# Kernel tuning notes

Hardware: AMD Instinct MI355X
Metric: run time of the kernel (lower is better)

Reference implementation:

```python
import jax, jax.numpy as jnp
import numpy as np
import math

D = 2048
H = 32
HKV = 8
HD = D // H
ROPE_BASE = 10000.0


def _rope_cache(T, hd, base=ROPE_BASE):
    theta = 1.0 / base ** (jnp.arange(0, hd, 2, dtype=jnp.float32) / hd)  # [hd//2]
    t = jnp.arange(T, dtype=jnp.float32)
    freqs = t[:, None] * theta[None, :]  # [T, hd//2]
    return jnp.cos(freqs), jnp.sin(freqs)


def _apply_rope(x, cos, sin):
    # x: [B, H, T, HD]; interleaved-pair rotation
    B, Hh, T, hd = x.shape
    x_ = x.reshape(B, Hh, T, hd // 2, 2)
    x1, x2 = x_[..., 0], x_[..., 1]
    c = cos[None, None, :, :]
    s = sin[None, None, :, :]
    rx1 = x1 * c - x2 * s
    rx2 = x1 * s + x2 * c
    return jnp.stack([rx1, rx2], axis=-1).reshape(B, Hh, T, hd)


def setup_inputs() -> dict:
    key = jax.random.key(0)
    ks = jax.random.split(key, 5)
    B, T = 1, 2048
    sc = 0.02
    return {
        "x": jax.random.normal(ks[0], (B, T, D), dtype=jnp.float32),
        "wq": jax.random.normal(ks[1], (D, D), dtype=jnp.float32) * sc,
        "wk": jax.random.normal(ks[2], (HKV * HD, D), dtype=jnp.float32) * sc,
        "wv": jax.random.normal(ks[3], (HKV * HD, D), dtype=jnp.float32) * sc,
        "wo": jax.random.normal(ks[4], (D, D), dtype=jnp.float32) * sc,
    }


def reference(x, wq, wk, wv, wo):
    B, T, _ = x.shape
    q = (x @ wq.T).reshape(B, T, H, HD).transpose(0, 2, 1, 3)      # [B,H,T,HD]
    k = (x @ wk.T).reshape(B, T, HKV, HD).transpose(0, 2, 1, 3)    # [B,HKV,T,HD]
    v = (x @ wv.T).reshape(B, T, HKV, HD).transpose(0, 2, 1, 3)

    cos, sin = _rope_cache(T, HD)
    q = _apply_rope(q, cos, sin)
    k = _apply_rope(k, cos, sin)

    rep = H // HKV
    k = jnp.repeat(k, rep, axis=1)  # repeat_interleave over head dim
    v = jnp.repeat(v, rep, axis=1)

    scores = jnp.einsum("bhtd,bhsd->bhts", q, k) / math.sqrt(HD)
    mask = jnp.triu(jnp.full((T, T), -jnp.inf, dtype=scores.dtype), k=1)
    scores = scores + mask[None, None, :, :]
    attn = jax.nn.softmax(scores, axis=-1)

    y = jnp.einsum("bhts,bhsd->bhtd", attn, v)
    y = y.transpose(0, 2, 1, 3).reshape(B, T, D)
    return y @ wo.T
```

## Files before the change

kernel.cpp:

```cpp
#include <hip/hip_runtime.h>
#include <hip/hip_bf16.h>
#include <cstdint>
#include <cstddef>

#define TT 2048
#define DDIM 2048
#define NH 32
#define NKV 8
#define HDIM 64

typedef __attribute__((ext_vector_type(8))) short bf16x8;
typedef __attribute__((ext_vector_type(4))) float f32x4;
typedef __attribute__((ext_vector_type(16))) float f32x16;

__device__ __forceinline__ unsigned short f2bf(float f) {
  unsigned u = __float_as_uint(f);
  unsigned r = 0x7FFFu + ((u >> 16) & 1u);
  return (unsigned short)((u + r) >> 16);
}
__device__ __forceinline__ float bf2f(unsigned short u) {
  return __uint_as_float((unsigned)u << 16);
}

__device__ __forceinline__ void gl_lds16(const void* g, void* l) {
  __builtin_amdgcn_global_load_lds(
      (const __attribute__((address_space(1))) void*)g,
      (__attribute__((address_space(3))) void*)l, 16, 0, 0);
}

__device__ __forceinline__ unsigned pkbf(float lo, float hi) {
  unsigned r;
  asm("v_cvt_pk_bf16_f32 %0, %1, %2" : "=v"(r) : "v"(lo), "v"(hi));
  return r;
}
__device__ __forceinline__ void swap32(unsigned& dst, unsigned& src) {
  asm volatile("v_permlane32_swap_b32 %0, %1" : "+v"(dst), "+v"(src));
}
union W4 { unsigned w[4]; bf16x8 v; };

__global__ __launch_bounds__(256)
void cast5_kernel(const float* __restrict__ x, const float* __restrict__ wq,
                  const float* __restrict__ wk, const float* __restrict__ wv,
                  const float* __restrict__ wo,
                  unsigned short* __restrict__ xb, unsigned short* __restrict__ wqb,
                  unsigned short* __restrict__ wkb, unsigned short* __restrict__ wvb,
                  unsigned short* __restrict__ wob) {
  int i = blockIdx.x * 256 + threadIdx.x;
  const float* s; unsigned short* d; int off;
  if (i < 1048576)      { s = x;  d = xb;  off = i; }
  else if (i < 2097152) { s = wq; d = wqb; off = i - 1048576; }
  else if (i < 2359296) { s = wk; d = wkb; off = i - 2097152; }
  else if (i < 2621440) { s = wv; d = wvb; off = i - 2359296; }
  else                  { s = wo; d = wob; off = i - 2621440; }
  float4 f = reinterpret_cast<const float4*>(s)[off];
  ushort4 o;
  o.x = f2bf(f.x); o.y = f2bf(f.y); o.z = f2bf(f.z); o.w = f2bf(f.w);
  reinterpret_cast<ushort4*>(d)[off] = o;
}

__device__ __forceinline__ void gemm64_body(
    const unsigned short* __restrict__ A, const unsigned short* __restrict__ B,
    int K, size_t arow, size_t brow,
    unsigned short (*As)[64 * 64], unsigned short (*Bs)[128 * 64],
    f32x4 (&acc)[2][4]) {
  const int tid = threadIdx.x;
  const int wave = tid >> 6, lane = tid & 63;
  const int wm = wave >> 1, wn = wave & 1;
  const int lr = lane & 15;
  const int gb = lane >> 4;
  const int srow = lane >> 3;
  const int scol = (((lane & 7) ^ srow) << 3);

#define G64_STAGE(buf, k0)                                                       \
  {                                                                              \
    for (int i = 0; i < 2; ++i) {                                                \
      int blk = wave * 2 + i;                                                    \
      int r = blk * 8 + srow;                                                    \
      gl_lds16(A + arow + (size_t)r * K + (k0) + scol, &As[buf][blk * 8 * 64]);  \
    }                                                                            \
    for (int i = 0; i < 4; ++i) {                                                \
      int blk = wave * 4 + i;                                                    \
      int r = blk * 8 + srow;                                                    \
      gl_lds16(B + brow + (size_t)r * K + (k0) + scol, &Bs[buf][blk * 8 * 64]);  \
    }                                                                            \
  }

  const int nt = K >> 6;
  G64_STAGE(0, 0)
  __syncthreads();
  int cur = 0;
  for (int t = 0; t < nt; ++t) {
    if (t + 1 < nt) { G64_STAGE(cur ^ 1, (t + 1) << 6) }

    bf16x8 af[2][2], bfr[2][4];
    for (int mi = 0; mi < 2; ++mi) {
      int row = wm * 32 + mi * 16 + lr, sw = row & 7;
      af[0][mi] = *reinterpret_cast<const bf16x8*>(&As[cur][row * 64 + ((gb ^ sw) << 3)]);
      af[1][mi] = *reinterpret_cast<const bf16x8*>(&As[cur][row * 64 + (((4 + gb) ^ sw) << 3)]);
    }
    for (int ni = 0; ni < 4; ++ni) {
      int row = wn * 64 + ni * 16 + lr, sw = row & 7;
      bfr[0][ni] = *reinterpret_cast<const bf16x8*>(&Bs[cur][row * 64 + ((gb ^ sw) << 3)]);
      bfr[1][ni] = *reinterpret_cast<const bf16x8*>(&Bs[cur][row * 64 + (((4 + gb) ^ sw) << 3)]);
    }
    __builtin_amdgcn_s_setprio(1);
    for (int kk = 0; kk < 2; ++kk)
      for (int mi = 0; mi < 2; ++mi)
        for (int ni = 0; ni < 4; ++ni)
          acc[mi][ni] = __builtin_amdgcn_mfma_f32_16x16x32_bf16(af[kk][mi], bfr[kk][ni], acc[mi][ni], 0, 0, 0);
    __builtin_amdgcn_s_setprio(0);
    __syncthreads();
    cur ^= 1;
  }
#undef G64_STAGE
}

__global__ __launch_bounds__(256, 3)
void qkv_fused_kernel(const unsigned short* __restrict__ xb,
                      const unsigned short* __restrict__ wqb,
                      const unsigned short* __restrict__ wkb,
                      const unsigned short* __restrict__ wvb,
                      unsigned short* __restrict__ qhb,
                      unsigned short* __restrict__ khb,
                      unsigned short* __restrict__ vtb) {
  __shared__ __align__(16) unsigned short As[2][64 * 64];
  __shared__ __align__(16) unsigned short Bs[2][128 * 64];
  const int bn = blockIdx.y;
  const unsigned short* B; int n0, mode;
  if (bn < 16)      { B = wqb; n0 = bn;      mode = 0; }
  else if (bn < 20) { B = wkb; n0 = bn - 16; mode = 1; }
  else              { B = wvb; n0 = bn - 20; mode = 2; }

  f32x4 acc[2][4];
  for (int i = 0; i < 2; ++i)
    for (int j = 0; j < 4; ++j)
      acc[i][j] = (f32x4){0.f, 0.f, 0.f, 0.f};

  gemm64_body(xb, B, 2048, (size_t)(blockIdx.x * 64) * 2048,
              (size_t)(n0 * 128) * 2048, As, Bs, acc);

  const int tid = threadIdx.x;
  const int wave = tid >> 6, lane = tid & 63;
  const int wm = wave >> 1, wn = wave & 1;
  const int lr = lane & 15;

  if (mode == 2) {
#pragma unroll
    for (int mi = 0; mi < 2; ++mi)
#pragma unroll
      for (int ni = 0; ni < 4; ++ni) {
        int n = n0 * 128 + wn * 64 + ni * 16 + lr;
        int tb = blockIdx.x * 64 + wm * 32 + mi * 16 + (lane >> 4) * 4;
        ushort4 u;
        u.x = f2bf(acc[mi][ni][0]); u.y = f2bf(acc[mi][ni][1]);
        u.z = f2bf(acc[mi][ni][2]); u.w = f2bf(acc[mi][ni][3]);
        *reinterpret_cast<ushort4*>(&vtb[(size_t)n * TT + tb]) = u;
      }
  } else {
    unsigned short* dst = (mode == 0) ? qhb : khb;
    const float scale = (mode == 0) ? 0.18033688011112042f : 1.0f;
#pragma unroll
    for (int mi = 0; mi < 2; ++mi)
#pragma unroll
      for (int ni = 0; ni < 4; ++ni) {
        int n = n0 * 128 + wn * 64 + ni * 16 + lr;
        int hh = n >> 6, d = n & 63, ii = d >> 1;
        float theta = exp2f(-(float)(2 * ii) * (13.287712379549449f / 64.0f));
        int tb = blockIdx.x * 64 + wm * 32 + mi * 16 + (lane >> 4) * 4;
#pragma unroll
        for (int r = 0; r < 4; ++r) {
          float self = acc[mi][ni][r];
          float part = __shfl_xor(self, 1);
          float sn, cs;
          __sincosf((float)(tb + r) * theta, &sn, &cs);
          float val = (d & 1) ? (part * sn + self * cs) : (self * cs - part * sn);
          dst[((size_t)hh * TT + tb + r) * HDIM + d] = f2bf(val * scale);
        }
      }
  }
}

__global__ __launch_bounds__(256, 3)
void out_gemm_kernel(const unsigned short* __restrict__ yb,
                     const unsigned short* __restrict__ wob,
                     float* __restrict__ out) {
  __shared__ __align__(16) unsigned short As[2][64 * 64];
  __shared__ __align__(16) unsigned short Bs[2][128 * 64];
  f32x4 acc[2][4];
  for (int i = 0; i < 2; ++i)
    for (int j = 0; j < 4; ++j)
      acc[i][j] = (f32x4){0.f, 0.f, 0.f, 0.f};

  gemm64_body(yb, wob, 2048, (size_t)(blockIdx.x * 64) * 2048,
              (size_t)(blockIdx.y * 128) * 2048, As, Bs, acc);

  const int tid = threadIdx.x;
  const int wave = tid >> 6, lane = tid & 63;
  const int wm = wave >> 1, wn = wave & 1;
  const int lr = lane & 15;
#pragma unroll
  for (int mi = 0; mi < 2; ++mi)
#pragma unroll
    for (int ni = 0; ni < 4; ++ni) {
      int col = blockIdx.y * 128 + wn * 64 + ni * 16 + lr;
      int rbase = blockIdx.x * 64 + wm * 32 + mi * 16 + (lane >> 4) * 4;
#pragma unroll
      for (int r = 0; r < 4; ++r)
        out[(size_t)(rbase + r) * DDIM + col] = acc[mi][ni][r];
    }
}

__global__ __launch_bounds__(256)
void attn_kernel(const unsigned short* __restrict__ qh,
                 const unsigned short* __restrict__ kh,
                 const unsigned short* __restrict__ vt,
                 unsigned short* __restrict__ po,
                 float* __restrict__ pm, float* __restrict__ pl) {
  __shared__ __align__(16) unsigned short Ks[2][64 * 64];
  __shared__ __align__(16) unsigned short Vts[2][64 * 64];
  const int kvg = blockIdx.x;
  const int by = blockIdx.y;
  const int qt = 63 - (by >> 1);
  const int par = by & 1;
  const int tid = threadIdx.x, wave = tid >> 6, lane = tid & 63;
  const int h = kvg * 4 + wave;
  const int qc = lane & 31, hi = lane >> 5;
  const int srow = lane >> 3;
  const int scol = (((lane & 7) ^ srow) << 3);

  bf16x8 qa[4];
  {
    const unsigned short* qrow = qh + ((size_t)h * TT + qt * 32 + qc) * HDIM + hi * 8;
#pragma unroll
    for (int ks = 0; ks < 4; ++ks)
      qa[ks] = *reinterpret_cast<const bf16x8*>(qrow + ks * 16);
  }

  f32x16 oA, oB;
#pragma unroll
  for (int r = 0; r < 16; ++r) { oA[r] = 0.f; oB[r] = 0.f; }
  float m_r = -1e30f, l_r = 0.f;

  const int njb = (qt >> 1) + 1;
  const int cnt = (njb - par + 1) >> 1;

#define A_STAGE(buf, jbx) do {                                                        \
    for (int i = 0; i < 2; ++i) {                                                     \
      int rblk = wave * 2 + i;                                                        \
      int rr = rblk * 8 + srow;                                                       \
      gl_lds16(kh + ((size_t)kvg * TT + (size_t)(jbx) * 64 + rr) * HDIM + scol,       \
               &Ks[buf][rblk * 8 * 64]);                                              \
      gl_lds16(vt + ((size_t)(kvg * HDIM + rr)) * TT + (size_t)(jbx) * 64 + scol,     \
               &Vts[buf][rblk * 8 * 64]);                                             \
    } } while (0)

  if (cnt > 0) {
    A_STAGE(0, par);
    __syncthreads();
    int cur = 0;

    for (int it = 0; it < cnt; ++it) {
      const int jb = par + 2 * it;
      if (it + 1 < cnt) A_STAGE(cur ^ 1, jb + 2);
      const bool diag = (jb == njb - 1);
      const bool hasB = (!diag) || (qt & 1);

      f32x16 stA, stB;
#pragma unroll
      for (int r = 0; r < 16; ++r) { stA[r] = 0.f; stB[r] = 0.f; }
      __builtin_amdgcn_s_setprio(1);
#pragma unroll
      for (int ks = 0; ks < 4; ++ks) {
        int row = qc, g = 2 * ks + hi;
        bf16x8 kf = *reinterpret_cast<const bf16x8*>(&Ks[cur][row * 64 + ((g ^ (row & 7)) << 3)]);
        stA = __builtin_amdgcn_mfma_f32_32x32x16_bf16(kf, qa[ks], stA, 0, 0, 0);
      }
      if (hasB) {
#pragma unroll
        for (int ks = 0; ks < 4; ++ks) {
          int row = 32 + qc, g = 2 * ks + hi;
          bf16x8 kf = *reinterpret_cast<const bf16x8*>(&Ks[cur][row * 64 + ((g ^ (row & 7)) << 3)]);
          stB = __builtin_amdgcn_mfma_f32_32x32x16_bf16(kf, qa[ks], stB, 0, 0, 0);
        }
      }
      __builtin_amdgcn_s_setprio(0);

      if (diag) {
        if (qt & 1) {
#pragma unroll
          for (int r = 0; r < 16; ++r) {
            int jloc = (r & 3) + 8 * (r >> 2) + 4 * hi;
            stB[r] = (jloc > qc) ? -1e30f : stB[r];
          }
        } else {
#pragma unroll
          for (int r = 0; r < 16; ++r) {
            int jloc = (r & 3) + 8 * (r >> 2) + 4 * hi;
            stA[r] = (jloc > qc) ? -1e30f : stA[r];
          }
        }
      }

      float pmx = stA[0];
#pragma unroll
      for (int r = 1; r < 16; ++r) pmx = fmaxf(pmx, stA[r]);
      if (hasB) {
#pragma unroll
        for (int r = 0; r < 16; ++r) pmx = fmaxf(pmx, stB[r]);
      }
      pmx = fmaxf(pmx, __shfl_xor(pmx, 32));
      if (!__all(pmx <= m_r + 12.f)) {
        float mn = fmaxf(m_r, pmx);
        float al = exp2f(m_r - mn);
        m_r = mn; l_r *= al;
#pragma unroll
        for (int r = 0; r < 16; ++r) {
          int qrow = (r & 3) + 8 * (r >> 2) + 4 * hi;
          float alr = __shfl(al, qrow);
          oA[r] *= alr; oB[r] *= alr;
        }
      }
      float sum = 0.f;
#pragma unroll
      for (int r = 0; r < 16; ++r) { stA[r] = exp2f(stA[r] - m_r); sum += stA[r]; }
      if (hasB) {
#pragma unroll
        for (int r = 0; r < 16; ++r) { stB[r] = exp2f(stB[r] - m_r); sum += stB[r]; }
      }
      sum += __shfl_xor(sum, 32);
      l_r += sum;

      W4 pf0, pf1, pf2, pf3;
#define REPACK(F0, F1, S)                                                   \
      F0.w[0] = pkbf(S[0], S[1]);  F0.w[1] = pkbf(S[2], S[3]);              \
      F0.w[2] = pkbf(S[4], S[5]);  F0.w[3] = pkbf(S[6], S[7]);              \
      swap32(F0.w[0], F0.w[2]);    swap32(F0.w[1], F0.w[3]);                \
      F1.w[0] = pkbf(S[8], S[9]);  F1.w[1] = pkbf(S[10], S[11]);            \
      F1.w[2] = pkbf(S[12], S[13]); F1.w[3] = pkbf(S[14], S[15]);           \
      swap32(F1.w[0], F1.w[2]);    swap32(F1.w[1], F1.w[3]);
      REPACK(pf0, pf1, stA)
      if (hasB) { REPACK(pf2, pf3, stB) }
#undef REPACK

      {
        const unsigned short* Vb = &Vts[cur][0];
        int r0 = qc, r1 = 32 + qc;
        int s0 = r0 & 7, s1 = r1 & 7;
        bf16x8 b;
        __builtin_amdgcn_s_setprio(1);
        b = *reinterpret_cast<const bf16x8*>(Vb + r0 * 64 + (((0 + hi) ^ s0) << 3));
        oA = __builtin_amdgcn_mfma_f32_32x32x16_bf16(pf0.v, b, oA, 0, 0, 0);
        b = *reinterpret_cast<const bf16x8*>(Vb + r1 * 64 + (((0 + hi) ^ s1) << 3));
        oB = __builtin_amdgcn_mfma_f32_32x32x16_bf16(pf0.v, b, oB, 0, 0, 0);
        b = *reinterpret_cast<const bf16x8*>(Vb + r0 * 64 + (((2 + hi) ^ s0) << 3));
        oA = __builtin_amdgcn_mfma_f32_32x32x16_bf16(pf1.v, b, oA, 0, 0, 0);
        b = *reinterpret_cast<const bf16x8*>(Vb + r1 * 64 + (((2 + hi) ^ s1) << 3));
        oB = __builtin_amdgcn_mfma_f32_32x32x16_bf16(pf1.v, b, oB, 0, 0, 0);
        if (hasB) {
          b = *reinterpret_cast<const bf16x8*>(Vb + r0 * 64 + (((4 + hi) ^ s0) << 3));
          oA = __builtin_amdgcn_mfma_f32_32x32x16_bf16(pf2.v, b, oA, 0, 0, 0);
          b = *reinterpret_cast<const bf16x8*>(Vb + r1 * 64 + (((4 + hi) ^ s1) << 3));
          oB = __builtin_amdgcn_mfma_f32_32x32x16_bf16(pf2.v, b, oB, 0, 0, 0);
          b = *reinterpret_cast<const bf16x8*>(Vb + r0 * 64 + (((6 + hi) ^ s0) << 3));
          oA = __builtin_amdgcn_mfma_f32_32x32x16_bf16(pf3.v, b, oA, 0, 0, 0);
          b = *reinterpret_cast<const bf16x8*>(Vb + r1 * 64 + (((6 + hi) ^ s1) << 3));
          oB = __builtin_amdgcn_mfma_f32_32x32x16_bf16(pf3.v, b, oB, 0, 0, 0);
        }
        __builtin_amdgcn_s_setprio(0);
      }
      __syncthreads();
      cur ^= 1;
    }
  }
#undef A_STAGE

  unsigned short* pop = po + (size_t)par * ((size_t)NH * TT * HDIM);
#pragma unroll
  for (int r = 0; r < 16; ++r) {
    int qrow = (r & 3) + 8 * (r >> 2) + 4 * hi;
    size_t base = ((size_t)h * TT + qt * 32 + qrow) * HDIM + qc;
    pop[base] = f2bf(oA[r]);
    pop[base + 32] = f2bf(oB[r]);
  }
  if (hi == 0) {
    size_t idx = ((size_t)par * NH + h) * TT + qt * 32 + qc;
    pm[idx] = m_r;
    pl[idx] = l_r;
  }
}

__global__ __launch_bounds__(256)
void attn_merge_kernel(const unsigned short* __restrict__ po,
                       const float* __restrict__ pm, const float* __restrict__ pl,
                       unsigned short* __restrict__ y) {
  int idx = blockIdx.x * 256 + threadIdx.x;
  int row = idx >> 4;
  int d0 = (idx & 15) << 2;
  int h = row >> 11, t = row & (TT - 1);
  const size_t P = (size_t)NH * TT * HDIM;
  const int NT = NH * TT;

  float m0 = pm[row], m1 = pm[NT + row];
  float l0 = pl[row], l1 = pl[NT + row];
  float M = fmaxf(m0, m1);
  float w0 = exp2f(m0 - M), w1 = exp2f(m1 - M);
  ushort4 u0 = *reinterpret_cast<const ushort4*>(&po[(size_t)row * HDIM + d0]);
  ushort4 u1 = *reinterpret_cast<const ushort4*>(&po[P + (size_t)row * HDIM + d0]);
  float inv = 1.0f / (w0 * l0 + w1 * l1);
  ushort4 o;
  o.x = f2bf((w0 * bf2f(u0.x) + w1 * bf2f(u1.x)) * inv);
  o.y = f2bf((w0 * bf2f(u0.y) + w1 * bf2f(u1.y)) * inv);
  o.z = f2bf((w0 * bf2f(u0.z) + w1 * bf2f(u1.z)) * inv);
  o.w = f2bf((w0 * bf2f(u0.w) + w1 * bf2f(u1.w)) * inv);
  *reinterpret_cast<ushort4*>(&y[(size_t)t * DDIM + h * HDIM + d0]) = o;
}

extern "C" void kernel_launch(void* const* d_in, const int* in_sizes, int n_in,
                              void* d_out, int out_size, void* d_ws, size_t ws_size,
                              hipStream_t stream) {
  const float* x  = (const float*)d_in[0];
  const float* wq = (const float*)d_in[1];
  const float* wk = (const float*)d_in[2];
  const float* wv = (const float*)d_in[3];
  const float* wo = (const float*)d_in[4];
  float* out = (float*)d_out;
  char* ws = (char*)d_ws;

  unsigned short* xb  = (unsigned short*)(ws + (size_t)0);
  unsigned short* wqb = (unsigned short*)(ws + ((size_t)8  << 20));
  unsigned short* wkb = (unsigned short*)(ws + ((size_t)16 << 20));
  unsigned short* wvb = (unsigned short*)(ws + ((size_t)18 << 20));
  unsigned short* wob = (unsigned short*)(ws + ((size_t)20 << 20));
  unsigned short* po  = (unsigned short*)(ws + ((size_t)28 << 20));
  float*          pm  = (float*)(ws + ((size_t)44 << 20));
  float*          pl  = (float*)(ws + ((size_t)45 << 20));
  unsigned short* qhb = (unsigned short*)(ws + ((size_t)52 << 20));
  unsigned short* khb = (unsigned short*)(ws + ((size_t)60 << 20));
  unsigned short* vtb = (unsigned short*)(ws + ((size_t)62 << 20));
  unsigned short* yb  = (unsigned short*)(ws + ((size_t)64 << 20));

  cast5_kernel<<<14336, 256, 0, stream>>>(x, wq, wk, wv, wo, xb, wqb, wkb, wvb, wob);

  qkv_fused_kernel<<<dim3(32, 24), 256, 0, stream>>>(xb, wqb, wkb, wvb, qhb, khb, vtb);

  attn_kernel<<<dim3(8, 128), 256, 0, stream>>>(qhb, khb, vtb, po, pm, pl);
  attn_merge_kernel<<<4096, 256, 0, stream>>>(po, pm, pl, yb);

  out_gemm_kernel<<<dim3(32, 16), 256, 0, stream>>>(yb, wob, out);
}
```

Before: 125.3 us.

## Remap GEMM block indices for L2 locality and switch softmax to natural exp

Both GEMM kernels now linearize the 2D block index and remap it with a stride-8 permutation, so blocks dispatched together share weight or activation tiles in cache. Separately, the Q scale drops the log2(e) factor (0.125 instead of 0.18) and the softmax and merge kernels use __expf instead of exp2f, with the rescale threshold lowered from 12 to 8. The math change keeps results equivalent but adds a multiply inside __expf, so it mostly trades cost. The remap assumes fixed grid shapes (96 and 64 blocks per group).

```diff
diff --git a/kernel.cpp b/kernel.cpp
--- a/kernel.cpp
+++ b/kernel.cpp
@@ -125,7 +125,11 @@
                       unsigned short* __restrict__ vtb) {
   __shared__ __align__(16) unsigned short As[2][64 * 64];
   __shared__ __align__(16) unsigned short Bs[2][128 * 64];
-  const int bn = blockIdx.y;
+  const int l = (int)(blockIdx.y * gridDim.x + blockIdx.x);
+  const int nl = (l & 7) * 96 + (l >> 3);
+  const int bx = nl & 31;
+  const int bn = nl >> 5;
+
   const unsigned short* B; int n0, mode;
   if (bn < 16)      { B = wqb; n0 = bn;      mode = 0; }
   else if (bn < 20) { B = wkb; n0 = bn - 16; mode = 1; }
@@ -136,7 +140,7 @@
     for (int j = 0; j < 4; ++j)
       acc[i][j] = (f32x4){0.f, 0.f, 0.f, 0.f};
 
-  gemm64_body(xb, B, 2048, (size_t)(blockIdx.x * 64) * 2048,
+  gemm64_body(xb, B, 2048, (size_t)(bx * 64) * 2048,
               (size_t)(n0 * 128) * 2048, As, Bs, acc);
 
   const int tid = threadIdx.x;
@@ -150,7 +154,7 @@
 #pragma unroll
       for (int ni = 0; ni < 4; ++ni) {
         int n = n0 * 128 + wn * 64 + ni * 16 + lr;
-        int tb = blockIdx.x * 64 + wm * 32 + mi * 16 + (lane >> 4) * 4;
+        int tb = bx * 64 + wm * 32 + mi * 16 + (lane >> 4) * 4;
         ushort4 u;
         u.x = f2bf(acc[mi][ni][0]); u.y = f2bf(acc[mi][ni][1]);
         u.z = f2bf(acc[mi][ni][2]); u.w = f2bf(acc[mi][ni][3]);
@@ -158,7 +162,7 @@
       }
   } else {
     unsigned short* dst = (mode == 0) ? qhb : khb;
-    const float scale = (mode == 0) ? 0.18033688011112042f : 1.0f;
+    const float scale = (mode == 0) ? 0.125f : 1.0f;
 #pragma unroll
     for (int mi = 0; mi < 2; ++mi)
 #pragma unroll
@@ -166,7 +170,7 @@
         int n = n0 * 128 + wn * 64 + ni * 16 + lr;
         int hh = n >> 6, d = n & 63, ii = d >> 1;
         float theta = exp2f(-(float)(2 * ii) * (13.287712379549449f / 64.0f));
-        int tb = blockIdx.x * 64 + wm * 32 + mi * 16 + (lane >> 4) * 4;
+        int tb = bx * 64 + wm * 32 + mi * 16 + (lane >> 4) * 4;
 #pragma unroll
         for (int r = 0; r < 4; ++r) {
           float self = acc[mi][ni][r];
@@ -186,13 +190,18 @@
                      float* __restrict__ out) {
   __shared__ __align__(16) unsigned short As[2][64 * 64];
   __shared__ __align__(16) unsigned short Bs[2][128 * 64];
+  const int l = (int)(blockIdx.y * gridDim.x + blockIdx.x);
+  const int nl = (l & 7) * 64 + (l >> 3);
+  const int bx = nl & 31;
+  const int by = nl >> 5;
+
   f32x4 acc[2][4];
   for (int i = 0; i < 2; ++i)
     for (int j = 0; j < 4; ++j)
       acc[i][j] = (f32x4){0.f, 0.f, 0.f, 0.f};
 
-  gemm64_body(yb, wob, 2048, (size_t)(blockIdx.x * 64) * 2048,
-              (size_t)(blockIdx.y * 128) * 2048, As, Bs, acc);
+  gemm64_body(yb, wob, 2048, (size_t)(bx * 64) * 2048,
+              (size_t)(by * 128) * 2048, As, Bs, acc);
 
   const int tid = threadIdx.x;
   const int wave = tid >> 6, lane = tid & 63;
@@ -202,8 +211,8 @@
   for (int mi = 0; mi < 2; ++mi)
 #pragma unroll
     for (int ni = 0; ni < 4; ++ni) {
-      int col = blockIdx.y * 128 + wn * 64 + ni * 16 + lr;
-      int rbase = blockIdx.x * 64 + wm * 32 + mi * 16 + (lane >> 4) * 4;
+      int col = by * 128 + wn * 64 + ni * 16 + lr;
+      int rbase = bx * 64 + wm * 32 + mi * 16 + (lane >> 4) * 4;
 #pragma unroll
       for (int r = 0; r < 4; ++r)
         out[(size_t)(rbase + r) * DDIM + col] = acc[mi][ni][r];
@@ -309,9 +318,9 @@
         for (int r = 0; r < 16; ++r) pmx = fmaxf(pmx, stB[r]);
       }
       pmx = fmaxf(pmx, __shfl_xor(pmx, 32));
-      if (!__all(pmx <= m_r + 12.f)) {
+      if (!__all(pmx <= m_r + 8.f)) {
         float mn = fmaxf(m_r, pmx);
-        float al = exp2f(m_r - mn);
+        float al = __expf(m_r - mn);
         m_r = mn; l_r *= al;
 #pragma unroll
         for (int r = 0; r < 16; ++r) {
@@ -322,10 +331,10 @@
       }
       float sum = 0.f;
 #pragma unroll
-      for (int r = 0; r < 16; ++r) { stA[r] = exp2f(stA[r] - m_r); sum += stA[r]; }
+      for (int r = 0; r < 16; ++r) { stA[r] = __expf(stA[r] - m_r); sum += stA[r]; }
       if (hasB) {
 #pragma unroll
-        for (int r = 0; r < 16; ++r) { stB[r] = exp2f(stB[r] - m_r); sum += stB[r]; }
+        for (int r = 0; r < 16; ++r) { stB[r] = __expf(stB[r] - m_r); sum += stB[r]; }
       }
       sum += __shfl_xor(sum, 32);
       l_r += sum;
@@ -403,7 +412,7 @@
   float m0 = pm[row], m1 = pm[NT + row];
   float l0 = pl[row], l1 = pl[NT + row];
   float M = fmaxf(m0, m1);
-  float w0 = exp2f(m0 - M), w1 = exp2f(m1 - M);
+  float w0 = __expf(m0 - M), w1 = __expf(m1 - M);
   ushort4 u0 = *reinterpret_cast<const ushort4*>(&po[(size_t)row * HDIM + d0]);
   ushort4 u1 = *reinterpret_cast<const ushort4*>(&po[P + (size_t)row * HDIM + d0]);
   float inv = 1.0f / (w0 * l0 + w1 * l1);
```

New measurement: 119.5 us. -4.6%, faster.
